# Optimization experiments

Hardware: AMD Instinct MI355X
Metric: run time of the kernel (lower is better)

Reference implementation:

```python
import jax, jax.numpy as jnp
import numpy as np

N_NODES = 100000
N_GRAPHS = 512
HID = 128
IN_DIM = 128
OUT_DIM = 10
N_EDGES = 1600000


def gcn_conv(x, src, dst, W, b, n):
    # PyG GCNConv: add self-loops, symmetric normalization D^-1/2 (A+I) D^-1/2, then linear.
    h = x @ W  # [N, H]
    deg = jnp.zeros((n,), h.dtype).at[dst].add(1.0) + 1.0  # +1 self-loop
    dinv = jax.lax.rsqrt(deg)
    norm = dinv[src] * dinv[dst]  # [E]
    agg = jnp.zeros_like(h).at[dst].add(h[src] * norm[:, None])
    agg = agg + h * (dinv * dinv)[:, None]  # self-loop messages
    return agg + b


def setup_inputs() -> dict:
    key = jax.random.key(0)
    ks = jax.random.split(key, 12)
    x = jax.random.normal(ks[0], (N_NODES, IN_DIM), jnp.float32)
    edge_index = jax.random.randint(ks[1], (2, N_EDGES), 0, N_NODES)
    batch = jnp.sort(jax.random.randint(ks[2], (N_NODES,), 0, N_GRAPHS))
    def lin(k, fan_in, shape):
        bound = 1.0 / np.sqrt(fan_in)
        return jax.random.uniform(k, shape, jnp.float32, -bound, bound)
    W1 = lin(ks[3], IN_DIM, (IN_DIM, HID)); b1 = lin(ks[4], IN_DIM, (HID,))
    W2 = lin(ks[5], HID, (HID, HID)); b2 = lin(ks[6], HID, (HID,))
    W3 = lin(ks[7], HID, (HID, HID)); b3 = lin(ks[8], HID, (HID,))
    Wc1 = lin(ks[9], 2 * HID, (2 * HID, HID)); bc1 = lin(ks[9], 2 * HID, (HID,))
    Wc2 = lin(ks[10], HID, (HID, OUT_DIM)); bc2 = lin(ks[11], HID, (OUT_DIM,))
    return {"x": x, "edge_index": edge_index, "batch": batch,
            "W1": W1, "b1": b1, "W2": W2, "b2": b2, "W3": W3, "b3": b3,
            "Wc1": Wc1, "bc1": bc1, "Wc2": Wc2, "bc2": bc2}


def reference(x, edge_index, batch, W1, b1, W2, b2, W3, b3, Wc1, bc1, Wc2, bc2):
    src, dst = edge_index[0], edge_index[1]
    n = x.shape[0]
    h = jax.nn.relu(gcn_conv(x, src, dst, W1, b1, n))
    h = jax.nn.relu(gcn_conv(h, src, dst, W2, b2, n))
    h = gcn_conv(h, src, dst, W3, b3, n)  # no relu after last conv
    # global mean pool
    sums = jax.ops.segment_sum(h, batch, num_segments=N_GRAPHS)
    cnt = jax.ops.segment_sum(jnp.ones((n,), h.dtype), batch, num_segments=N_GRAPHS)
    mean = sums / jnp.maximum(cnt, 1.0)[:, None]
    # global max pool
    mx = jax.ops.segment_max(h, batch, num_segments=N_GRAPHS)
    mx = jnp.where(jnp.isfinite(mx), mx, 0.0)
    g = jnp.concatenate([mean, mx], axis=1)  # [G, 2H]
    g = jax.nn.relu(g @ Wc1 + bc1)
    return g @ Wc2 + bc2
```

## Files before the change

kernel.cpp:

```cpp
#include <hip/hip_runtime.h>

#define H 128
#define CAP 64

typedef __attribute__((ext_vector_type(8))) short bf16x8;
typedef __attribute__((ext_vector_type(4))) float f32x4;

__device__ __forceinline__ unsigned short f2bf(float f) {
  unsigned u = __float_as_uint(f);
  unsigned r = u + 0x7FFFu + ((u >> 16) & 1u);
  return (unsigned short)(r >> 16);
}
__device__ __forceinline__ float bf2f(unsigned short s) {
  return __uint_as_float(((unsigned)s) << 16);
}

__global__ __launch_bounds__(256) void setup_all(
    const float* __restrict__ x,
    const float* __restrict__ W1, const float* __restrict__ W2, const float* __restrict__ W3,
    unsigned short* __restrict__ Xb, unsigned short* __restrict__ Wt,
    int* __restrict__ csr_src, int cap4,
    unsigned short* __restrict__ P, unsigned short* __restrict__ Q,
    int* __restrict__ cursor, int cur4,
    int n, int totalX4) {
  long long i = (long long)blockIdx.x * 256 + threadIdx.x;
  if (i < totalX4) {
    float4 v = *(const float4*)(x + i * 4);
    ushort4 o;
    o.x = f2bf(v.x); o.y = f2bf(v.y); o.z = f2bf(v.z); o.w = f2bf(v.w);
    *(ushort4*)(Xb + i * 4) = o;
    return;
  }
  i -= totalX4;
  if (i < cap4) {
    *(int4*)(csr_src + i * 4) = make_int4(n, n, n, n);
    return;
  }
  i -= cap4;
  if (i < 3 * H * H) {
    int w = (int)(i >> 14);
    int rem = (int)i & (H * H - 1);
    int c = rem >> 7;
    int k = rem & 127;
    const float* W = (w == 0) ? W1 : (w == 1) ? W2 : W3;
    Wt[i] = f2bf(W[(size_t)k * H + c]);
    return;
  }
  i -= 3 * H * H;
  if (i < cur4) {
    *(int4*)(cursor + i * 4) = make_int4(0, 0, 0, 0);
    return;
  }
  i -= cur4;
  if (i < H) {
    P[(size_t)n * H + i] = 0;
    Q[(size_t)n * H + i] = 0;
  }
}

__global__ __launch_bounds__(256) void csr_fill_fixed(
    const int* __restrict__ src, const int* __restrict__ dst,
    int* __restrict__ cursor, int* __restrict__ csr_src,
    int ne, int range, int slices) {
  int r = blockIdx.x & 7;
  int slice = blockIdx.x >> 3;
  int ne4 = ne / 4;
  int chunk4 = (ne4 + slices - 1) / slices;
  int beg4 = slice * chunk4;
  int end4 = beg4 + chunk4; if (end4 > ne4) end4 = ne4;
  int lo = r * range;
  int hi = lo + range;
  for (int e4 = beg4 + threadIdx.x; e4 < end4; e4 += 256) {
    int e = e4 * 4;
    int4 d = *(const int4*)(dst + e);
    if (d.x >= lo && d.x < hi) { int p = atomicAdd(&cursor[d.x], 1); if (p < CAP) csr_src[(size_t)d.x * CAP + p] = src[e + 0]; }
    if (d.y >= lo && d.y < hi) { int p = atomicAdd(&cursor[d.y], 1); if (p < CAP) csr_src[(size_t)d.y * CAP + p] = src[e + 1]; }
    if (d.z >= lo && d.z < hi) { int p = atomicAdd(&cursor[d.z], 1); if (p < CAP) csr_src[(size_t)d.z * CAP + p] = src[e + 2]; }
    if (d.w >= lo && d.w < hi) { int p = atomicAdd(&cursor[d.w], 1); if (p < CAP) csr_src[(size_t)d.w * CAP + p] = src[e + 3]; }
  }
  if (r == 0 && slice == 0) {
    int base = ne4 * 4;
    int t = base + threadIdx.x;
    if (t < ne) {
      int d = dst[t];
      int p = atomicAdd(&cursor[d], 1);
      if (p < CAP) csr_src[(size_t)d * CAP + p] = src[t];
    }
  }
}

__global__ void dinv_gstart(const int* __restrict__ deg, float* __restrict__ dinv,
                            const int* __restrict__ batch, int* __restrict__ g_start,
                            int n, int G) {
  int i = blockIdx.x * blockDim.x + threadIdx.x;
  if (i >= n) return;
  dinv[i] = rsqrtf((float)(deg[i] + 1));
  int b = batch[i];
  int prev = (i == 0) ? -1 : batch[i - 1];
  for (int g = prev + 1; g <= b; ++g) g_start[g] = i;
  if (i == n - 1) {
    for (int g = b + 1; g <= G; ++g) g_start[g] = n;
  }
}

#define SWLD 136
__global__ __launch_bounds__(256) void gemm_mfma(
    const unsigned short* __restrict__ Ab, const unsigned short* __restrict__ Wt,
    const float* __restrict__ dinv, unsigned short* __restrict__ outb, int n) {
  __shared__ unsigned short sW[H * SWLD];
  int tid = threadIdx.x;
  {
    int c = tid >> 1, hh = tid & 1;
    const int4* s = (const int4*)(Wt + (size_t)c * H + hh * 64);
    int4* d = (int4*)(sW + (size_t)c * SWLD + hh * 64);
#pragma unroll
    for (int i = 0; i < 8; ++i) d[i] = s[i];
  }
  __syncthreads();

  int wave = tid >> 6;
  int lane = tid & 63;
  int m = lane & 15;
  int quad = lane >> 4;
  int row = blockIdx.x * 64 + wave * 16 + m;
  bool rv = row < n;

  f32x4 acc[8];
#pragma unroll
  for (int t = 0; t < 8; ++t) acc[t] = (f32x4){0.f, 0.f, 0.f, 0.f};

  const unsigned short* arow = Ab + (size_t)(rv ? row : 0) * H;
#pragma unroll
  for (int k0 = 0; k0 < H; k0 += 32) {
    bf16x8 af;
    if (rv) af = *(const bf16x8*)(arow + k0 + quad * 8);
    else    af = (bf16x8){0, 0, 0, 0, 0, 0, 0, 0};
#pragma unroll
    for (int ct = 0; ct < 8; ++ct) {
      bf16x8 bfr = *(const bf16x8*)(sW + (size_t)(ct * 16 + m) * SWLD + k0 + quad * 8);
      acc[ct] = __builtin_amdgcn_mfma_f32_16x16x32_bf16(af, bfr, acc[ct], 0, 0, 0);
    }
  }

  int orow0 = blockIdx.x * 64 + wave * 16 + quad * 4;
#pragma unroll
  for (int r = 0; r < 4; ++r) {
    int orow = orow0 + r;
    if (orow < n) {
      float dv = dinv[orow];
      unsigned short* o = outb + (size_t)orow * H + m;
#pragma unroll
      for (int ct = 0; ct < 8; ++ct) o[ct * 16] = f2bf(acc[ct][r] * dv);
    }
  }
}

template <bool RELU, bool OUTF32>
__global__ __launch_bounds__(256) void aggregate_bf(
    const unsigned short* __restrict__ hs, const int* __restrict__ deg,
    const int* __restrict__ csr_src, const float* __restrict__ dinv,
    const float* __restrict__ b, void* __restrict__ outv, int n) {
  int node = blockIdx.x * 8 + (threadIdx.x >> 5);
  if (node >= n) return;
  int c = (threadIdx.x & 31) << 2;
  int beg = node * CAP;
  int end = beg + ((deg[node] + 7) & ~7);

  ushort4 sv = *(const ushort4*)(hs + (size_t)node * H + c);
  float4 acc;
  acc.x = bf2f(sv.x); acc.y = bf2f(sv.y); acc.z = bf2f(sv.z); acc.w = bf2f(sv.w);

  int4 ia, ib;
  if (beg < end) {
    ia = *(const int4*)(csr_src + beg);
    ib = *(const int4*)(csr_src + beg + 4);
  }
  for (int k = beg; k < end; k += 8) {
    int4 ca = ia, cb = ib;
    int kn = k + 8;
    if (kn < end) {
      ia = *(const int4*)(csr_src + kn);
      ib = *(const int4*)(csr_src + kn + 4);
    }
    ushort4 v0 = *(const ushort4*)(hs + (size_t)ca.x * H + c);
    ushort4 v1 = *(const ushort4*)(hs + (size_t)ca.y * H + c);
    ushort4 v2 = *(const ushort4*)(hs + (size_t)ca.z * H + c);
    ushort4 v3 = *(const ushort4*)(hs + (size_t)ca.w * H + c);
    ushort4 v4 = *(const ushort4*)(hs + (size_t)cb.x * H + c);
    ushort4 v5 = *(const ushort4*)(hs + (size_t)cb.y * H + c);
    ushort4 v6 = *(const ushort4*)(hs + (size_t)cb.z * H + c);
    ushort4 v7 = *(const ushort4*)(hs + (size_t)cb.w * H + c);
    acc.x += ((bf2f(v0.x) + bf2f(v1.x)) + (bf2f(v2.x) + bf2f(v3.x))) +
             ((bf2f(v4.x) + bf2f(v5.x)) + (bf2f(v6.x) + bf2f(v7.x)));
    acc.y += ((bf2f(v0.y) + bf2f(v1.y)) + (bf2f(v2.y) + bf2f(v3.y))) +
             ((bf2f(v4.y) + bf2f(v5.y)) + (bf2f(v6.y) + bf2f(v7.y)));
    acc.z += ((bf2f(v0.z) + bf2f(v1.z)) + (bf2f(v2.z) + bf2f(v3.z))) +
             ((bf2f(v4.z) + bf2f(v5.z)) + (bf2f(v6.z) + bf2f(v7.z)));
    acc.w += ((bf2f(v0.w) + bf2f(v1.w)) + (bf2f(v2.w) + bf2f(v3.w))) +
             ((bf2f(v4.w) + bf2f(v5.w)) + (bf2f(v6.w) + bf2f(v7.w)));
  }

  float dv = dinv[node];
  float4 bb = *(const float4*)(b + c);
  float4 o;
  o.x = fmaf(acc.x, dv, bb.x);
  o.y = fmaf(acc.y, dv, bb.y);
  o.z = fmaf(acc.z, dv, bb.z);
  o.w = fmaf(acc.w, dv, bb.w);
  if (RELU) {
    o.x = fmaxf(o.x, 0.f); o.y = fmaxf(o.y, 0.f);
    o.z = fmaxf(o.z, 0.f); o.w = fmaxf(o.w, 0.f);
  }
  if (OUTF32) {
    *(float4*)((float*)outv + (size_t)node * H + c) = o;
  } else {
    ushort4 ob;
    ob.x = f2bf(o.x); ob.y = f2bf(o.y); ob.z = f2bf(o.z); ob.w = f2bf(o.w);
    *(ushort4*)((unsigned short*)outv + (size_t)node * H + c) = ob;
  }
}

__global__ __launch_bounds__(256) void pool2(
    const float* __restrict__ h, const int* __restrict__ g_start,
    float* __restrict__ gmean, float* __restrict__ gmax, int n) {
  __shared__ float ssum[16][64];
  __shared__ float smax[16][64];
  int g = blockIdx.x >> 1;
  int half = blockIdx.x & 1;
  int beg = g_start[g];
  int end = g_start[g + 1];
  int q = threadIdx.x >> 4;
  int c = (threadIdx.x & 15) << 2;
  int cg = half * 64 + c;

  float4 s = make_float4(0.f, 0.f, 0.f, 0.f);
  float4 m = make_float4(-INFINITY, -INFINITY, -INFINITY, -INFINITY);
  for (int node = beg + q; node < end; node += 16) {
    float4 v = *(const float4*)(h + (size_t)node * H + cg);
    s.x += v.x; s.y += v.y; s.z += v.z; s.w += v.w;
    m.x = fmaxf(m.x, v.x); m.y = fmaxf(m.y, v.y);
    m.z = fmaxf(m.z, v.z); m.w = fmaxf(m.w, v.w);
  }
  *(float4*)&ssum[q][c] = s;
  *(float4*)&smax[q][c] = m;
  __syncthreads();

  int cnt = end - beg;
  int t = threadIdx.x;
  if (t < 64) {
    float tot = 0.f;
#pragma unroll
    for (int qq = 0; qq < 16; ++qq) tot += ssum[qq][t];
    gmean[(size_t)g * H + half * 64 + t] = tot / fmaxf((float)cnt, 1.0f);
  } else if (t < 128) {
    int cc = t - 64;
    float mx = -INFINITY;
#pragma unroll
    for (int qq = 0; qq < 16; ++qq) mx = fmaxf(mx, smax[qq][cc]);
    gmax[(size_t)g * H + half * 64 + cc] = (cnt == 0) ? 0.0f : mx;
  }
}

__global__ __launch_bounds__(128) void classify_kernel(
    const float* __restrict__ gmean, const float* __restrict__ gmax,
    const float* __restrict__ Wc1, const float* __restrict__ bc1,
    const float* __restrict__ Wc2, const float* __restrict__ bc2,
    float* __restrict__ out) {
  __shared__ float gv[2 * H];
  __shared__ float hid[H];
  int gid = blockIdx.x;
  int t = threadIdx.x;
  gv[t] = gmean[(size_t)gid * H + t];
  gv[H + t] = gmax[(size_t)gid * H + t];
  __syncthreads();
  float acc = 0.f;
#pragma unroll 8
  for (int k = 0; k < 2 * H; ++k) acc = fmaf(gv[k], Wc1[(size_t)k * H + t], acc);
  hid[t] = fmaxf(acc + bc1[t], 0.f);
  __syncthreads();
  if (t < 10) {
    float a2 = 0.f;
    for (int j = 0; j < H; ++j) a2 = fmaf(hid[j], Wc2[(size_t)j * 10 + t], a2);
    out[(size_t)gid * 10 + t] = a2 + bc2[t];
  }
}

extern "C" void kernel_launch(void* const* d_in, const int* in_sizes, int n_in,
                              void* d_out, int out_size, void* d_ws, size_t ws_size,
                              hipStream_t stream) {
  const float* x    = (const float*)d_in[0];
  const int* ei     = (const int*)d_in[1];
  const int* batch  = (const int*)d_in[2];
  const float* W1   = (const float*)d_in[3];
  const float* b1   = (const float*)d_in[4];
  const float* W2   = (const float*)d_in[5];
  const float* b2   = (const float*)d_in[6];
  const float* W3   = (const float*)d_in[7];
  const float* b3   = (const float*)d_in[8];
  const float* Wc1  = (const float*)d_in[9];
  const float* bc1  = (const float*)d_in[10];
  const float* Wc2  = (const float*)d_in[11];
  const float* bc2  = (const float*)d_in[12];
  float* out = (float*)d_out;

  const int n  = in_sizes[2];
  const int ne = in_sizes[1] / 2;
  const int G  = 512;
  const size_t NFb = (size_t)(n + 1) * H;

  const int* src = ei;
  const int* dst = ei + ne;

  unsigned short* P_bf = (unsigned short*)d_ws;
  unsigned short* Q_bf = P_bf + NFb;
  float*          F2f  = (float*)(Q_bf + NFb);
  unsigned short* Xb   = (unsigned short*)F2f;
  int* csr_src = (int*)(F2f + (size_t)n * H);
  const size_t csr_cap = (size_t)n * CAP;
  char* p = (char*)(csr_src + csr_cap);
  int*            cursor   = (int*)p;            p += (size_t)n * 4;
  float*          dinv     = (float*)p;          p += (size_t)n * 4;
  int*            g_start  = (int*)p;            p += (size_t)(G + 1) * 4;
  float*          gmean    = (float*)p;          p += (size_t)G * H * 4;
  float*          gmax     = (float*)p;          p += (size_t)G * H * 4;
  p = (char*)(((uintptr_t)p + 255) & ~(uintptr_t)255);
  unsigned short* Wt       = (unsigned short*)p; p += (size_t)3 * H * H * 2;

  {
    int totalX4 = n * H / 4;
    int cap4 = (int)(csr_cap / 4);
    int cur4 = n / 4;
    long long tot = (long long)totalX4 + cap4 + 3 * H * H + cur4 + H;
    int blocks = (int)((tot + 255) / 256);
    setup_all<<<blocks, 256, 0, stream>>>(x, W1, W2, W3, Xb, Wt, csr_src, cap4,
                                          P_bf, Q_bf, cursor, cur4, n, totalX4);
  }

  int range = (n + 7) / 8;
  csr_fill_fixed<<<128 * 8, 256, 0, stream>>>(src, dst, cursor, csr_src, ne, range, 128);
  dinv_gstart<<<(n + 255) / 256, 256, 0, stream>>>(cursor, dinv, batch, g_start, n, G);

  const int tile_grid = (n + 63) / 64;
  const int node_grid = (n + 7) / 8;

  gemm_mfma<<<tile_grid, 256, 0, stream>>>(Xb, Wt, dinv, Q_bf, n);
  aggregate_bf<true, false><<<node_grid, 256, 0, stream>>>(Q_bf, cursor, csr_src, dinv, b1, P_bf, n);

  gemm_mfma<<<tile_grid, 256, 0, stream>>>(P_bf, Wt + H * H, dinv, Q_bf, n);
  aggregate_bf<true, false><<<node_grid, 256, 0, stream>>>(Q_bf, cursor, csr_src, dinv, b2, P_bf, n);

  gemm_mfma<<<tile_grid, 256, 0, stream>>>(P_bf, Wt + 2 * H * H, dinv, Q_bf, n);
  aggregate_bf<false, true><<<node_grid, 256, 0, stream>>>(Q_bf, cursor, csr_src, dinv, b3, F2f, n);

  pool2<<<2 * G, 256, 0, stream>>>(F2f, g_start, gmean, gmax, n);
  classify_kernel<<<G, 128, 0, stream>>>(gmean, gmax, Wc1, bc1, Wc2, bc2, out);
}
```

Measured before the change: 457.0 us.

## Bucket edges by destination range before CSR fill; drop CSR padding init

Replaces the CSR fill, in which every block scanned all edges for each of 8 destination ranges, with a two-pass scheme. The first pass scatters (src,dst) pairs into 8 range buckets using block-local counts and one global atomic per bucket. The second pass places each bucket's edges through per-node cursor atomics. It also removes the full padding init of csr_src by masking unused slots to the zero row inside aggregation. The aim is to cut the 8x redundant reads of dst and the large memset of the CSR array, at the cost of an extra kernel, writes to a bucket buffer aliased onto Q, and a fixed bucket capacity that could overflow on skewed inputs.

```diff
diff --git a/kernel.cpp b/kernel.cpp
--- a/kernel.cpp
+++ b/kernel.cpp
@@ -2,6 +2,7 @@
 
 #define H 128
 #define CAP 64
+#define BCAP 262144
 
 typedef __attribute__((ext_vector_type(8))) short bf16x8;
 typedef __attribute__((ext_vector_type(4))) float f32x4;
@@ -19,9 +20,8 @@
     const float* __restrict__ x,
     const float* __restrict__ W1, const float* __restrict__ W2, const float* __restrict__ W3,
     unsigned short* __restrict__ Xb, unsigned short* __restrict__ Wt,
-    int* __restrict__ csr_src, int cap4,
     unsigned short* __restrict__ P, unsigned short* __restrict__ Q,
-    int* __restrict__ cursor, int cur4,
+    int* __restrict__ cursor, int cur4, int* __restrict__ bcount,
     int n, int totalX4) {
   long long i = (long long)blockIdx.x * 256 + threadIdx.x;
   if (i < totalX4) {
@@ -32,11 +32,6 @@
     return;
   }
   i -= totalX4;
-  if (i < cap4) {
-    *(int4*)(csr_src + i * 4) = make_int4(n, n, n, n);
-    return;
-  }
-  i -= cap4;
   if (i < 3 * H * H) {
     int w = (int)(i >> 14);
     int rem = (int)i & (H * H - 1);
@@ -55,37 +50,78 @@
   if (i < H) {
     P[(size_t)n * H + i] = 0;
     Q[(size_t)n * H + i] = 0;
-  }
-}
-
-__global__ __launch_bounds__(256) void csr_fill_fixed(
+    return;
+  }
+  i -= H;
+  if (i < 8) bcount[i] = 0;
+}
+
+__global__ __launch_bounds__(256) void bucket_edges(
     const int* __restrict__ src, const int* __restrict__ dst,
-    int* __restrict__ cursor, int* __restrict__ csr_src,
-    int ne, int range, int slices) {
+    int2* __restrict__ buckets, int* __restrict__ bcount,
+    int ne, float invr) {
+  __shared__ int cnt[8];
+  __shared__ int gbase[8];
+  int tid = threadIdx.x;
+  if (tid < 8) cnt[tid] = 0;
+  __syncthreads();
+
+  int ne4 = ne >> 2;
+  int e4 = blockIdx.x * 256 + tid;
+  bool valid = e4 < ne4;
+  int4 s4, d4;
+  int r0 = 0, r1 = 0, r2 = 0, r3 = 0;
+  int l0 = 0, l1 = 0, l2 = 0, l3 = 0;
+  if (valid) {
+    s4 = *(const int4*)(src + e4 * 4);
+    d4 = *(const int4*)(dst + e4 * 4);
+    int t;
+    t = (int)((float)d4.x * invr); r0 = t < 0 ? 0 : (t > 7 ? 7 : t);
+    t = (int)((float)d4.y * invr); r1 = t < 0 ? 0 : (t > 7 ? 7 : t);
+    t = (int)((float)d4.z * invr); r2 = t < 0 ? 0 : (t > 7 ? 7 : t);
+    t = (int)((float)d4.w * invr); r3 = t < 0 ? 0 : (t > 7 ? 7 : t);
+    l0 = atomicAdd(&cnt[r0], 1);
+    l1 = atomicAdd(&cnt[r1], 1);
+    l2 = atomicAdd(&cnt[r2], 1);
+    l3 = atomicAdd(&cnt[r3], 1);
+  }
+  __syncthreads();
+  if (tid < 8) gbase[tid] = atomicAdd(&bcount[tid], cnt[tid]);
+  __syncthreads();
+  if (valid) {
+    int p0 = gbase[r0] + l0;
+    int p1 = gbase[r1] + l1;
+    int p2 = gbase[r2] + l2;
+    int p3 = gbase[r3] + l3;
+    if (p0 < BCAP) buckets[(r0 << 18) + p0] = make_int2(s4.x, d4.x);
+    if (p1 < BCAP) buckets[(r1 << 18) + p1] = make_int2(s4.y, d4.y);
+    if (p2 < BCAP) buckets[(r2 << 18) + p2] = make_int2(s4.z, d4.z);
+    if (p3 < BCAP) buckets[(r3 << 18) + p3] = make_int2(s4.w, d4.w);
+  }
+  if (blockIdx.x == 0 && tid < (ne & 3)) {
+    int e = ne4 * 4 + tid;
+    int d = dst[e];
+    int t = (int)((float)d * invr);
+    int rr = t < 0 ? 0 : (t > 7 ? 7 : t);
+    int p = atomicAdd(&bcount[rr], 1);
+    if (p < BCAP) buckets[(rr << 18) + p] = make_int2(src[e], d);
+  }
+}
+
+__global__ __launch_bounds__(256) void place_edges(
+    const int2* __restrict__ buckets, const int* __restrict__ bcount,
+    int* __restrict__ cursor, int* __restrict__ csr_src, int slices) {
   int r = blockIdx.x & 7;
-  int slice = blockIdx.x >> 3;
-  int ne4 = ne / 4;
-  int chunk4 = (ne4 + slices - 1) / slices;
-  int beg4 = slice * chunk4;
-  int end4 = beg4 + chunk4; if (end4 > ne4) end4 = ne4;
-  int lo = r * range;
-  int hi = lo + range;
-  for (int e4 = beg4 + threadIdx.x; e4 < end4; e4 += 256) {
-    int e = e4 * 4;
-    int4 d = *(const int4*)(dst + e);
-    if (d.x >= lo && d.x < hi) { int p = atomicAdd(&cursor[d.x], 1); if (p < CAP) csr_src[(size_t)d.x * CAP + p] = src[e + 0]; }
-    if (d.y >= lo && d.y < hi) { int p = atomicAdd(&cursor[d.y], 1); if (p < CAP) csr_src[(size_t)d.y * CAP + p] = src[e + 1]; }
-    if (d.z >= lo && d.z < hi) { int p = atomicAdd(&cursor[d.z], 1); if (p < CAP) csr_src[(size_t)d.z * CAP + p] = src[e + 2]; }
-    if (d.w >= lo && d.w < hi) { int p = atomicAdd(&cursor[d.w], 1); if (p < CAP) csr_src[(size_t)d.w * CAP + p] = src[e + 3]; }
-  }
-  if (r == 0 && slice == 0) {
-    int base = ne4 * 4;
-    int t = base + threadIdx.x;
-    if (t < ne) {
-      int d = dst[t];
-      int p = atomicAdd(&cursor[d], 1);
-      if (p < CAP) csr_src[(size_t)d * CAP + p] = src[t];
-    }
+  int s = blockIdx.x >> 3;
+  int cnt = bcount[r]; if (cnt > BCAP) cnt = BCAP;
+  int chunk = (cnt + slices - 1) / slices;
+  int beg = s * chunk;
+  int end = beg + chunk; if (end > cnt) end = cnt;
+  const int2* b = buckets + ((size_t)r << 18);
+  for (int i = beg + threadIdx.x; i < end; i += 256) {
+    int2 e = b[i];
+    int p = atomicAdd(&cursor[e.y], 1);
+    if (p < CAP) csr_src[(size_t)e.y * CAP + p] = e.x;
   }
 }
 
@@ -157,14 +193,15 @@
 
 template <bool RELU, bool OUTF32>
 __global__ __launch_bounds__(256) void aggregate_bf(
-    const unsigned short* __restrict__ hs, const int* __restrict__ deg,
+    const unsigned short* __restrict__ hs, const int* __restrict__ deg_,
     const int* __restrict__ csr_src, const float* __restrict__ dinv,
     const float* __restrict__ b, void* __restrict__ outv, int n) {
   int node = blockIdx.x * 8 + (threadIdx.x >> 5);
   if (node >= n) return;
   int c = (threadIdx.x & 31) << 2;
+  int deg = deg_[node]; if (deg > CAP) deg = CAP;
   int beg = node * CAP;
-  int end = beg + ((deg[node] + 7) & ~7);
+  int end = beg + ((deg + 7) & ~7);
 
   ushort4 sv = *(const ushort4*)(hs + (size_t)node * H + c);
   float4 acc;
@@ -181,6 +218,17 @@
     if (kn < end) {
       ia = *(const int4*)(csr_src + kn);
       ib = *(const int4*)(csr_src + kn + 4);
+    }
+    int rk = k - beg;
+    if (rk + 8 > deg) {
+      ca.x = (rk + 0 < deg) ? ca.x : n;
+      ca.y = (rk + 1 < deg) ? ca.y : n;
+      ca.z = (rk + 2 < deg) ? ca.z : n;
+      ca.w = (rk + 3 < deg) ? ca.w : n;
+      cb.x = (rk + 4 < deg) ? cb.x : n;
+      cb.y = (rk + 5 < deg) ? cb.y : n;
+      cb.z = (rk + 6 < deg) ? cb.z : n;
+      cb.w = (rk + 7 < deg) ? cb.w : n;
     }
     ushort4 v0 = *(const ushort4*)(hs + (size_t)ca.x * H + c);
     ushort4 v1 = *(const ushort4*)(hs + (size_t)ca.y * H + c);
@@ -325,19 +373,23 @@
   float*          gmax     = (float*)p;          p += (size_t)G * H * 4;
   p = (char*)(((uintptr_t)p + 255) & ~(uintptr_t)255);
   unsigned short* Wt       = (unsigned short*)p; p += (size_t)3 * H * H * 2;
+  int*            bcount   = (int*)p;            p += 32;
+  int2*           buckets  = (int2*)Q_bf;
 
   {
     int totalX4 = n * H / 4;
-    int cap4 = (int)(csr_cap / 4);
     int cur4 = n / 4;
-    long long tot = (long long)totalX4 + cap4 + 3 * H * H + cur4 + H;
+    long long tot = (long long)totalX4 + 3 * H * H + cur4 + H + 8;
     int blocks = (int)((tot + 255) / 256);
-    setup_all<<<blocks, 256, 0, stream>>>(x, W1, W2, W3, Xb, Wt, csr_src, cap4,
-                                          P_bf, Q_bf, cursor, cur4, n, totalX4);
+    setup_all<<<blocks, 256, 0, stream>>>(x, W1, W2, W3, Xb, Wt,
+                                          P_bf, Q_bf, cursor, cur4, bcount, n, totalX4);
   }
 
   int range = (n + 7) / 8;
-  csr_fill_fixed<<<128 * 8, 256, 0, stream>>>(src, dst, cursor, csr_src, ne, range, 128);
+  float invr = 1.0f / (float)range;
+  int bblocks = (ne / 4 + 255) / 256;
+  bucket_edges<<<bblocks, 256, 0, stream>>>(src, dst, buckets, bcount, ne, invr);
+  place_edges<<<8 * 256, 256, 0, stream>>>(buckets, bcount, cursor, csr_src, 256);
   dinv_gstart<<<(n + 255) / 256, 256, 0, stream>>>(cursor, dinv, batch, g_start, n, G);
 
   const int tile_grid = (n + 63) / 64;
```

Result: slower. 471.6 us (+3.2%).
